# Performance work log

Measured on AMD Instinct MI355X. Metric: run time of the kernel, lower is better.

Reference implementation:

```python
import jax, jax.numpy as jnp
import numpy as np

N_RAYS = 131072
N_NODES = 524288
ENC_DEPTH = 8
ENC_DIM = 16
N_POINTS = 8
IN_DIM = N_POINTS * ENC_DEPTH * ENC_DIM  # 1024
INNER = 64


def setup_inputs() -> dict:
    key = jax.random.key(0)
    ks = jax.random.split(key, 9)
    orig = jax.random.uniform(ks[0], (N_RAYS, 3), dtype=jnp.float32)
    end = jax.random.uniform(ks[1], (N_RAYS, 3), dtype=jnp.float32)
    history = jax.random.randint(ks[2], (N_RAYS, ENC_DEPTH), 0, N_NODES, dtype=jnp.int32).astype(jnp.int64)
    nodes_min = jax.random.uniform(ks[3], (N_NODES, 3), dtype=jnp.float32)
    # extents strictly positive (module replaces 0 extents with 0.5)
    nodes_extent = jax.random.uniform(ks[4], (N_NODES, 3), dtype=jnp.float32) + 0.1
    emb = jax.random.normal(ks[5], (N_NODES, 8 * ENC_DIM), dtype=jnp.float32) * 0.1
    W1 = jax.random.normal(ks[6], (IN_DIM, INNER), dtype=jnp.float32) * (1.0 / np.sqrt(IN_DIM))
    W2 = jax.random.normal(ks[7], (INNER, INNER), dtype=jnp.float32) * (1.0 / np.sqrt(INNER))
    W3 = jax.random.normal(ks[8], (INNER, 2), dtype=jnp.float32) * (1.0 / np.sqrt(INNER))
    return {"orig": orig, "end": end, "history": history, "nodes_min": nodes_min,
            "nodes_extent": nodes_extent, "emb": emb, "W1": W1, "W2": W2, "W3": W3}


def _net_forward(orig, end, history, nodes_min, nodes_extent, emb, W1, W2, W3):
    n = orig.shape[0]
    d = history.shape[1]
    # gather per-ray, per-depth node data (irregular access)
    nmin = nodes_min[history]          # (n, d, 3)
    ext = nodes_extent[history]        # (n, d, 3)
    po = jnp.clip((orig[:, None, :] - nmin) / ext, 0.0, 1.0)  # (n, d, 3)
    pe = jnp.clip((end[:, None, :] - nmin) / ext, 0.0, 1.0)
    ts = jnp.linspace(0.0, 1.0, N_POINTS, dtype=orig.dtype)
    pts = po[:, :, None, :] + (pe - po)[:, :, None, :] * ts[None, None, :, None]  # (n, d, P, 3)
    xd, yd, zd = pts[..., 0], pts[..., 1], pts[..., 2]
    # corner weights in the same order as bbox_feature.chunk(8): 000,100,010,001,101,011,110,111
    w = jnp.stack([
        (1 - xd) * (1 - yd) * (1 - zd),
        xd * (1 - yd) * (1 - zd),
        (1 - xd) * yd * (1 - zd),
        (1 - xd) * (1 - yd) * zd,
        xd * (1 - yd) * zd,
        (1 - xd) * yd * zd,
        xd * yd * (1 - zd),
        xd * yd * zd,
    ], axis=-1)                                    # (n, d, P, 8)
    corners = emb[history].reshape(n, d, 8, ENC_DIM)  # (n, d, 8, F)
    feat = jnp.einsum('ndpk,ndkf->ndpf', w, corners)  # (n, d, P, F)
    feat = feat.reshape(n, d * N_POINTS * ENC_DIM)    # concat over depth
    h = jax.nn.relu(feat @ W1)
    h = jax.nn.relu(h @ W2)
    a = h @ W3                                        # (n, 2)
    lengths = jnp.linalg.norm(end - orig, axis=-1)
    pred_cls = a[:, 0]
    pred_dist = a[:, 1] * lengths
    return jnp.stack([pred_cls, pred_dist], axis=-1)  # (n, 2)


def reference(orig, end, history, nodes_min, nodes_extent, emb, W1, W2, W3):
    return _net_forward(orig, end, history, nodes_min, nodes_extent, emb, W1, W2, W3)
```

## Files before the change

### kernel.cpp

```cpp
#include <hip/hip_runtime.h>
#include <cstdint>
#include <type_traits>

#define ENC_DEPTH 8
#define RAYS 64
#define THREADS 256

typedef __attribute__((ext_vector_type(8))) short bf16x8;
typedef __attribute__((ext_vector_type(4))) float f32x4;

__device__ __forceinline__ unsigned short f2bf(float x) {
    union { float f; unsigned u; } v; v.f = x;
    unsigned r = v.u + 0x7fffu + ((v.u >> 16) & 1u);
    return (unsigned short)(r >> 16);
}
__device__ __forceinline__ float bf2f(unsigned short h) {
    union { unsigned u; float f; } v; v.u = ((unsigned)h) << 16;
    return v.f;
}
__device__ __forceinline__ float clamp01(float x) {
    return fminf(fmaxf(x, 0.0f), 1.0f);
}
__device__ __forceinline__ void async_copy16(const void* g, void* l) {
    __builtin_amdgcn_global_load_lds(
        (const __attribute__((address_space(1))) void*)g,
        (__attribute__((address_space(3))) void*)l, 16, 0, 0);
}

__global__ void emb_bf16_kernel(const float* __restrict__ emb,
                                unsigned short* __restrict__ emb2) {
    size_t i = ((size_t)blockIdx.x * 256 + threadIdx.x) * 8;
    float4 a = *(const float4*)(emb + i);
    float4 b = *(const float4*)(emb + i + 4);
    bf16x8 v;
    v[0] = (short)f2bf(a.x); v[1] = (short)f2bf(a.y);
    v[2] = (short)f2bf(a.z); v[3] = (short)f2bf(a.w);
    v[4] = (short)f2bf(b.x); v[5] = (short)f2bf(b.y);
    v[6] = (short)f2bf(b.z); v[7] = (short)f2bf(b.w);
    *(bf16x8*)(emb2 + i) = v;
}

__global__ void w1_frag_kernel(const float* __restrict__ W1,
                               unsigned short* __restrict__ W1F) {
    int slot = blockIdx.x * 256 + threadIdx.x;
    int lane = slot & 63, tile = (slot >> 6) & 3, kk = (slot >> 8) & 3, d = slot >> 10;
    int n = tile * 16 + (lane & 15);
    int kbase = d * 128 + kk * 32 + (lane >> 4) * 8;
    bf16x8 v;
    #pragma unroll
    for (int j = 0; j < 8; ++j) v[j] = (short)f2bf(W1[(size_t)(kbase + j) * 64 + n]);
    *(bf16x8*)(W1F + (size_t)slot * 8) = v;
}

template <int BF16T>
__global__ __launch_bounds__(THREADS) void nbvh3(
    const float* __restrict__ orig, const float* __restrict__ endp,
    const int* __restrict__ hist, const float* __restrict__ nodes_min,
    const float* __restrict__ nodes_extent, const void* __restrict__ embx,
    const unsigned short* __restrict__ W1F, const float* __restrict__ W2,
    const float* __restrict__ W3, float* __restrict__ out)
{
    using CTy = typename std::conditional<BF16T, unsigned short, float>::type;
    __shared__ __align__(16) CTy cbuf[2][8320];
    __shared__ float pope_s[RAYS * ENC_DEPTH * 6];
    __shared__ int hist_s[RAYS * ENC_DEPTH];

    const int t = threadIdx.x;
    const int lane = t & 63, w = t >> 6;
    const int r0 = blockIdx.x * RAYS;

    hist_s[t] = hist[r0 * ENC_DEPTH + t];
    hist_s[t + 256] = hist[r0 * ENC_DEPTH + t + 256];
    __syncthreads();

    auto issue_gather = [&](int d, int buf) {
        char* base = (char*)&cbuf[buf][0];
        if (BF16T) {
            #pragma unroll
            for (int r = 0; r < 4; ++r) {
                int ray = r * 16 + w * 4 + (lane >> 4);
                int node = hist_s[(ray << 3) + d];
                const char* g = (const char*)embx + ((size_t)node << 8) + ((lane & 15) << 4);
                async_copy16(g, base + (r * 4 + w) * 1040 + lane * 16);
            }
        } else {
            #pragma unroll
            for (int r = 0; r < 8; ++r) {
                int ray = r * 8 + w * 2 + (lane >> 5);
                int node = hist_s[(ray << 3) + d];
                const char* g = (const char*)embx + ((size_t)node << 9) + ((lane & 31) << 4);
                async_copy16(g, base + (r * 4 + w) * 1040 + lane * 16);
            }
        }
    };

    issue_gather(0, 0);

    #pragma unroll
    for (int rep = 0; rep < 2; ++rep) {
        int task = t + rep * 256;
        int ray = task >> 3;
        int node = hist_s[task];
        float nm0 = nodes_min[node * 3 + 0], nm1 = nodes_min[node * 3 + 1], nm2 = nodes_min[node * 3 + 2];
        float ex0 = nodes_extent[node * 3 + 0], ex1 = nodes_extent[node * 3 + 1], ex2 = nodes_extent[node * 3 + 2];
        float o0 = orig[(r0 + ray) * 3 + 0], o1 = orig[(r0 + ray) * 3 + 1], o2 = orig[(r0 + ray) * 3 + 2];
        float e0 = endp[(r0 + ray) * 3 + 0], e1 = endp[(r0 + ray) * 3 + 1], e2 = endp[(r0 + ray) * 3 + 2];
        float* pp = pope_s + task * 6;
        pp[0] = clamp01((o0 - nm0) / ex0);
        pp[1] = clamp01((o1 - nm1) / ex1);
        pp[2] = clamp01((o2 - nm2) / ex2);
        pp[3] = clamp01((e0 - nm0) / ex0);
        pp[4] = clamp01((e1 - nm1) / ex1);
        pp[5] = clamp01((e2 - nm2) / ex2);
    }
    __syncthreads();

    f32x4 acc[4];
    #pragma unroll
    for (int i = 0; i < 4; ++i) acc[i] = (f32x4){0.f, 0.f, 0.f, 0.f};

    const int c = lane & 15, q = lane >> 4;
    const int ray = w * 16 + c;
    const int qh = q & 1;
    const int qp = q >> 1;

    #pragma unroll 1
    for (int d = 0; d < ENC_DEPTH; ++d) {
        if (d < ENC_DEPTH - 1) issue_gather(d + 1, (d + 1) & 1);

        bf16x8 bfr[4][4];
        #pragma unroll
        for (int kk = 0; kk < 4; ++kk)
            #pragma unroll
            for (int tile = 0; tile < 4; ++tile)
                bfr[kk][tile] = *(const bf16x8*)(W1F +
                    ((size_t)(((d * 4 + kk) * 4 + tile) * 64 + lane)) * 8);

        const float* pp = pope_s + ((ray << 3) + d) * 6;
        float po0 = pp[0], po1 = pp[1], po2 = pp[2], pe0 = pp[3], pe1 = pp[4], pe2 = pp[5];
        float X[4], OX[4], Y[4], OY[4], Z[4], OZ[4];
        #pragma unroll
        for (int kk = 0; kk < 4; ++kk) {
            float tp = (float)(2 * kk + qp) * (1.0f / 7.0f);
            X[kk] = po0 + (pe0 - po0) * tp; OX[kk] = 1.f - X[kk];
            Y[kk] = po1 + (pe1 - po1) * tp; OY[kk] = 1.f - Y[kk];
            Z[kk] = po2 + (pe2 - po2) * tp; OZ[kk] = 1.f - Z[kk];
        }

        float fa[4][8];
        #pragma unroll
        for (int kk = 0; kk < 4; ++kk)
            #pragma unroll
            for (int j = 0; j < 8; ++j) fa[kk][j] = 0.f;

        #pragma unroll
        for (int j = 0; j < 8; ++j) {
            int c8 = j ^ (c & 3);
            float e[8];
            if (BF16T) {
                const unsigned short* crow = (const unsigned short*)&cbuf[d & 1][0]
                    + (ray >> 2) * 520 + (ray & 3) * 128 + c8 * 16 + qh * 8;
                bf16x8 cv = *(const bf16x8*)crow;
                #pragma unroll
                for (int i = 0; i < 8; ++i) e[i] = bf2f((unsigned short)cv[i]);
            } else {
                const float* crow = (const float*)&cbuf[d & 1][0]
                    + (ray >> 1) * 260 + (ray & 1) * 128 + c8 * 16 + qh * 8;
                float4 ea = *(const float4*)crow;
                float4 eb = *(const float4*)(crow + 4);
                e[0] = ea.x; e[1] = ea.y; e[2] = ea.z; e[3] = ea.w;
                e[4] = eb.x; e[5] = eb.y; e[6] = eb.z; e[7] = eb.w;
            }
            #pragma unroll
            for (int kk = 0; kk < 4; ++kk) {
                float wx = ((0xD2 >> c8) & 1) ? X[kk] : OX[kk];
                float wy = ((0xE4 >> c8) & 1) ? Y[kk] : OY[kk];
                float wz = ((0xB8 >> c8) & 1) ? Z[kk] : OZ[kk];
                float wgt = wx * wy * wz;
                #pragma unroll
                for (int i = 0; i < 8; ++i)
                    fa[kk][i] = fmaf(wgt, e[i], fa[kk][i]);
            }
        }

        #pragma unroll
        for (int kk = 0; kk < 4; ++kk) {
            bf16x8 af;
            #pragma unroll
            for (int j = 0; j < 8; ++j) af[j] = (short)f2bf(fa[kk][j]);
            #pragma unroll
            for (int tile = 0; tile < 4; ++tile)
                acc[tile] = __builtin_amdgcn_mfma_f32_16x16x32_bf16(af, bfr[kk][tile], acc[tile], 0, 0, 0);
        }
        __syncthreads();
    }

    float* h1 = (float*)&cbuf[0][0];
    float* h2 = BF16T ? ((float*)&cbuf[1][0]) : (((float*)&cbuf[0][0]) + 4160);
    #pragma unroll
    for (int tile = 0; tile < 4; ++tile)
        #pragma unroll
        for (int r = 0; r < 4; ++r)
            h1[(w * 16 + q * 4 + r) * 65 + tile * 16 + c] = fmaxf(acc[tile][r], 0.f);
    __syncthreads();

    {
        int ray2 = t >> 2, jg = (t & 3) << 4;
        float s[16];
        #pragma unroll
        for (int j = 0; j < 16; ++j) s[j] = 0.f;
        const float* hrow = h1 + ray2 * 65;
        #pragma unroll 4
        for (int i = 0; i < 64; ++i) {
            float hv = hrow[i];
            const float4* wr = (const float4*)(W2 + (i << 6) + jg);
            float4 a0 = wr[0], a1 = wr[1], a2 = wr[2], a3 = wr[3];
            s[0]  = fmaf(hv, a0.x, s[0]);  s[1]  = fmaf(hv, a0.y, s[1]);
            s[2]  = fmaf(hv, a0.z, s[2]);  s[3]  = fmaf(hv, a0.w, s[3]);
            s[4]  = fmaf(hv, a1.x, s[4]);  s[5]  = fmaf(hv, a1.y, s[5]);
            s[6]  = fmaf(hv, a1.z, s[6]);  s[7]  = fmaf(hv, a1.w, s[7]);
            s[8]  = fmaf(hv, a2.x, s[8]);  s[9]  = fmaf(hv, a2.y, s[9]);
            s[10] = fmaf(hv, a2.z, s[10]); s[11] = fmaf(hv, a2.w, s[11]);
            s[12] = fmaf(hv, a3.x, s[12]); s[13] = fmaf(hv, a3.y, s[13]);
            s[14] = fmaf(hv, a3.z, s[14]); s[15] = fmaf(hv, a3.w, s[15]);
        }
        float* h2row = h2 + ray2 * 65 + jg;
        #pragma unroll
        for (int j = 0; j < 16; ++j) h2row[j] = fmaxf(s[j], 0.f);
    }
    __syncthreads();

    if (t < 128) {
        int ray3 = t >> 1, cc = t & 1;
        const float* hrow = h2 + ray3 * 65;
        float a = 0.f;
        #pragma unroll 16
        for (int i = 0; i < 64; ++i) a = fmaf(hrow[i], W3[i * 2 + cc], a);
        if (cc) {
            float dx = endp[(r0 + ray3) * 3 + 0] - orig[(r0 + ray3) * 3 + 0];
            float dy = endp[(r0 + ray3) * 3 + 1] - orig[(r0 + ray3) * 3 + 1];
            float dz = endp[(r0 + ray3) * 3 + 2] - orig[(r0 + ray3) * 3 + 2];
            a *= sqrtf(dx * dx + dy * dy + dz * dz);
        }
        out[((r0 + ray3) << 1) + cc] = a;
    }
}

extern "C" void kernel_launch(void* const* d_in, const int* in_sizes, int n_in,
                              void* d_out, int out_size, void* d_ws, size_t ws_size,
                              hipStream_t stream) {
    const float* orig = (const float*)d_in[0];
    const float* endp = (const float*)d_in[1];
    const int*   hist = (const int*)d_in[2];
    const float* nmin = (const float*)d_in[3];
    const float* next = (const float*)d_in[4];
    const float* emb  = (const float*)d_in[5];
    const float* W1   = (const float*)d_in[6];
    const float* W2   = (const float*)d_in[7];
    const float* W3   = (const float*)d_in[8];
    float* out = (float*)d_out;

    const int n_nodes = in_sizes[5] / 128;
    const size_t emb2_bytes = (size_t)n_nodes * 128 * 2;
    const int n_rays = in_sizes[0] / 3;
    const bool use_bf16 = ws_size >= emb2_bytes + 131072 * 2;

    if (use_bf16) {
        unsigned short* EMB2 = (unsigned short*)d_ws;
        unsigned short* W1F = (unsigned short*)((char*)d_ws + emb2_bytes);
        emb_bf16_kernel<<<dim3((n_nodes * 128) / (256 * 8)), dim3(256), 0, stream>>>(emb, EMB2);
        w1_frag_kernel<<<dim3(32), dim3(256), 0, stream>>>(W1, W1F);
        nbvh3<1><<<dim3(n_rays / RAYS), dim3(THREADS), 0, stream>>>(
            orig, endp, hist, nmin, next, EMB2, W1F, W2, W3, out);
    } else {
        unsigned short* W1F = (unsigned short*)d_ws;
        w1_frag_kernel<<<dim3(32), dim3(256), 0, stream>>>(W1, W1F);
        nbvh3<0><<<dim3(n_rays / RAYS), dim3(THREADS), 0, stream>>>(
            orig, endp, hist, nmin, next, emb, W1F, W2, W3, out);
    }
}
```

Measured before the change: 601.1 us.

## Make gather pipeline wave-private with 4-stage buffering and vmcnt waits

Each wave now loads its own 16 rays' history and node data, and gathers its own embedding rows into a wave-private slice of a 4-deep LDS ring. This removes every block-wide __syncthreads in the depth loop and replaces them with s_waitcnt vmcnt waits. Two depths are processed per iteration, with W1 fragments for both loaded up front and the gathers for the next two depths issued two steps ahead. The fp32 fallback is dropped and launch_bounds(256,2) is added, which costs more LDS and register pressure and assumes the workspace is always large enough.

New measurement: 665.6 us. 10.7% more time.

```diff
diff --git a/kernel.cpp b/kernel.cpp
--- a/kernel.cpp
+++ b/kernel.cpp
@@ -1,6 +1,5 @@
 #include <hip/hip_runtime.h>
 #include <cstdint>
-#include <type_traits>
 
 #define ENC_DEPTH 8
 #define RAYS 64
@@ -26,6 +25,9 @@
         (const __attribute__((address_space(1))) void*)g,
         (__attribute__((address_space(3))) void*)l, 16, 0, 0);
 }
+
+#define WAIT_VMCNT_8() __builtin_amdgcn_s_waitcnt(0xF78)
+#define WAIT_VMCNT_0() __builtin_amdgcn_s_waitcnt(0xF70)
 
 __global__ void emb_bf16_kernel(const float* __restrict__ emb,
                                 unsigned short* __restrict__ emb2) {
@@ -52,16 +54,14 @@
     *(bf16x8*)(W1F + (size_t)slot * 8) = v;
 }
 
-template <int BF16T>
-__global__ __launch_bounds__(THREADS) void nbvh3(
+__global__ __launch_bounds__(THREADS, 2) void nbvh4(
     const float* __restrict__ orig, const float* __restrict__ endp,
     const int* __restrict__ hist, const float* __restrict__ nodes_min,
-    const float* __restrict__ nodes_extent, const void* __restrict__ embx,
+    const float* __restrict__ nodes_extent, const unsigned short* __restrict__ EMB2,
     const unsigned short* __restrict__ W1F, const float* __restrict__ W2,
     const float* __restrict__ W3, float* __restrict__ out)
 {
-    using CTy = typename std::conditional<BF16T, unsigned short, float>::type;
-    __shared__ __align__(16) CTy cbuf[2][8320];
+    __shared__ __align__(16) unsigned short cbuf[33280];
     __shared__ float pope_s[RAYS * ENC_DEPTH * 6];
     __shared__ int hist_s[RAYS * ENC_DEPTH];
 
@@ -69,74 +69,60 @@
     const int lane = t & 63, w = t >> 6;
     const int r0 = blockIdx.x * RAYS;
 
-    hist_s[t] = hist[r0 * ENC_DEPTH + t];
-    hist_s[t + 256] = hist[r0 * ENC_DEPTH + t + 256];
-    __syncthreads();
-
-    auto issue_gather = [&](int d, int buf) {
-        char* base = (char*)&cbuf[buf][0];
-        if (BF16T) {
-            #pragma unroll
-            for (int r = 0; r < 4; ++r) {
-                int ray = r * 16 + w * 4 + (lane >> 4);
-                int node = hist_s[(ray << 3) + d];
-                const char* g = (const char*)embx + ((size_t)node << 8) + ((lane & 15) << 4);
-                async_copy16(g, base + (r * 4 + w) * 1040 + lane * 16);
-            }
-        } else {
-            #pragma unroll
-            for (int r = 0; r < 8; ++r) {
-                int ray = r * 8 + w * 2 + (lane >> 5);
-                int node = hist_s[(ray << 3) + d];
-                const char* g = (const char*)embx + ((size_t)node << 9) + ((lane & 31) << 4);
-                async_copy16(g, base + (r * 4 + w) * 1040 + lane * 16);
-            }
-        }
-    };
-
-    issue_gather(0, 0);
-
+    hist_s[w * 128 + lane]      = hist[(r0 + w * 16) * 8 + lane];
+    hist_s[w * 128 + 64 + lane] = hist[(r0 + w * 16) * 8 + 64 + lane];
+
+    float pv[2][6];
+    int tasks[2];
     #pragma unroll
     for (int rep = 0; rep < 2; ++rep) {
-        int task = t + rep * 256;
-        int ray = task >> 3;
-        int node = hist_s[task];
+        int task = rep * 64 + lane;
+        tasks[rep] = task;
+        int rw = task >> 3;
+        int node = hist_s[w * 128 + task];
         float nm0 = nodes_min[node * 3 + 0], nm1 = nodes_min[node * 3 + 1], nm2 = nodes_min[node * 3 + 2];
         float ex0 = nodes_extent[node * 3 + 0], ex1 = nodes_extent[node * 3 + 1], ex2 = nodes_extent[node * 3 + 2];
-        float o0 = orig[(r0 + ray) * 3 + 0], o1 = orig[(r0 + ray) * 3 + 1], o2 = orig[(r0 + ray) * 3 + 2];
-        float e0 = endp[(r0 + ray) * 3 + 0], e1 = endp[(r0 + ray) * 3 + 1], e2 = endp[(r0 + ray) * 3 + 2];
-        float* pp = pope_s + task * 6;
-        pp[0] = clamp01((o0 - nm0) / ex0);
-        pp[1] = clamp01((o1 - nm1) / ex1);
-        pp[2] = clamp01((o2 - nm2) / ex2);
-        pp[3] = clamp01((e0 - nm0) / ex0);
-        pp[4] = clamp01((e1 - nm1) / ex1);
-        pp[5] = clamp01((e2 - nm2) / ex2);
-    }
-    __syncthreads();
+        int gr = r0 + w * 16 + rw;
+        float o0 = orig[gr * 3 + 0], o1 = orig[gr * 3 + 1], o2 = orig[gr * 3 + 2];
+        float e0 = endp[gr * 3 + 0], e1 = endp[gr * 3 + 1], e2 = endp[gr * 3 + 2];
+        pv[rep][0] = clamp01((o0 - nm0) / ex0);
+        pv[rep][1] = clamp01((o1 - nm1) / ex1);
+        pv[rep][2] = clamp01((o2 - nm2) / ex2);
+        pv[rep][3] = clamp01((e0 - nm0) / ex0);
+        pv[rep][4] = clamp01((e1 - nm1) / ex1);
+        pv[rep][5] = clamp01((e2 - nm2) / ex2);
+    }
+
+    auto issue_depth = [&](int d) {
+        char* base = (char*)cbuf + (d & 3) * 16640 + w * 4160;
+        #pragma unroll
+        for (int r = 0; r < 4; ++r) {
+            int rw = r * 4 + (lane >> 4);
+            int node = hist_s[w * 128 + rw * 8 + d];
+            const char* g = (const char*)EMB2 + ((size_t)node << 8) + ((lane & 15) << 4);
+            async_copy16(g, base + r * 1040 + lane * 16);
+        }
+    };
+    issue_depth(0);
+    issue_depth(1);
+
+    #pragma unroll
+    for (int rep = 0; rep < 2; ++rep) {
+        float* pp = pope_s + w * 768 + tasks[rep] * 6;
+        #pragma unroll
+        for (int i = 0; i < 6; ++i) pp[i] = pv[rep][i];
+    }
 
     f32x4 acc[4];
     #pragma unroll
     for (int i = 0; i < 4; ++i) acc[i] = (f32x4){0.f, 0.f, 0.f, 0.f};
 
     const int c = lane & 15, q = lane >> 4;
-    const int ray = w * 16 + c;
     const int qh = q & 1;
     const int qp = q >> 1;
 
-    #pragma unroll 1
-    for (int d = 0; d < ENC_DEPTH; ++d) {
-        if (d < ENC_DEPTH - 1) issue_gather(d + 1, (d + 1) & 1);
-
-        bf16x8 bfr[4][4];
-        #pragma unroll
-        for (int kk = 0; kk < 4; ++kk)
-            #pragma unroll
-            for (int tile = 0; tile < 4; ++tile)
-                bfr[kk][tile] = *(const bf16x8*)(W1F +
-                    ((size_t)(((d * 4 + kk) * 4 + tile) * 64 + lane)) * 8);
-
-        const float* pp = pope_s + ((ray << 3) + d) * 6;
+    auto compute_depth = [&](int d, const bf16x8* bfr) {
+        const float* pp = pope_s + w * 768 + (c * 8 + d) * 6;
         float po0 = pp[0], po1 = pp[1], po2 = pp[2], pe0 = pp[3], pe1 = pp[4], pe2 = pp[5];
         float X[4], OX[4], Y[4], OY[4], Z[4], OZ[4];
         #pragma unroll
@@ -146,31 +132,21 @@
             Y[kk] = po1 + (pe1 - po1) * tp; OY[kk] = 1.f - Y[kk];
             Z[kk] = po2 + (pe2 - po2) * tp; OZ[kk] = 1.f - Z[kk];
         }
-
         float fa[4][8];
         #pragma unroll
         for (int kk = 0; kk < 4; ++kk)
             #pragma unroll
             for (int j = 0; j < 8; ++j) fa[kk][j] = 0.f;
 
+        const char* cb = (const char*)cbuf + (d & 3) * 16640 + w * 4160
+                         + (c >> 2) * 1040 + (c & 3) * 256 + qh * 16;
         #pragma unroll
         for (int j = 0; j < 8; ++j) {
             int c8 = j ^ (c & 3);
+            bf16x8 cv = *(const bf16x8*)(cb + c8 * 32);
             float e[8];
-            if (BF16T) {
-                const unsigned short* crow = (const unsigned short*)&cbuf[d & 1][0]
-                    + (ray >> 2) * 520 + (ray & 3) * 128 + c8 * 16 + qh * 8;
-                bf16x8 cv = *(const bf16x8*)crow;
-                #pragma unroll
-                for (int i = 0; i < 8; ++i) e[i] = bf2f((unsigned short)cv[i]);
-            } else {
-                const float* crow = (const float*)&cbuf[d & 1][0]
-                    + (ray >> 1) * 260 + (ray & 1) * 128 + c8 * 16 + qh * 8;
-                float4 ea = *(const float4*)crow;
-                float4 eb = *(const float4*)(crow + 4);
-                e[0] = ea.x; e[1] = ea.y; e[2] = ea.z; e[3] = ea.w;
-                e[4] = eb.x; e[5] = eb.y; e[6] = eb.z; e[7] = eb.w;
-            }
+            #pragma unroll
+            for (int i = 0; i < 8; ++i) e[i] = bf2f((unsigned short)cv[i]);
             #pragma unroll
             for (int kk = 0; kk < 4; ++kk) {
                 float wx = ((0xD2 >> c8) & 1) ? X[kk] : OX[kk];
@@ -182,7 +158,6 @@
                     fa[kk][i] = fmaf(wgt, e[i], fa[kk][i]);
             }
         }
-
         #pragma unroll
         for (int kk = 0; kk < 4; ++kk) {
             bf16x8 af;
@@ -190,13 +165,26 @@
             for (int j = 0; j < 8; ++j) af[j] = (short)f2bf(fa[kk][j]);
             #pragma unroll
             for (int tile = 0; tile < 4; ++tile)
-                acc[tile] = __builtin_amdgcn_mfma_f32_16x16x32_bf16(af, bfr[kk][tile], acc[tile], 0, 0, 0);
-        }
-        __syncthreads();
-    }
-
-    float* h1 = (float*)&cbuf[0][0];
-    float* h2 = BF16T ? ((float*)&cbuf[1][0]) : (((float*)&cbuf[0][0]) + 4160);
+                acc[tile] = __builtin_amdgcn_mfma_f32_16x16x32_bf16(af, bfr[kk * 4 + tile], acc[tile], 0, 0, 0);
+        }
+    };
+
+    #pragma unroll 1
+    for (int dd = 0; dd < 8; dd += 2) {
+        bf16x8 bfr[2][16];
+        #pragma unroll
+        for (int h = 0; h < 2; ++h)
+            #pragma unroll
+            for (int f = 0; f < 16; ++f)
+                bfr[h][f] = *(const bf16x8*)(W1F + ((size_t)(((dd + h) * 16 + f) * 64 + lane)) * 8);
+        if (dd + 2 < 8) { issue_depth(dd + 2); issue_depth(dd + 3); }
+        if (dd < 6) WAIT_VMCNT_8(); else WAIT_VMCNT_0();
+        compute_depth(dd, bfr[0]);
+        compute_depth(dd + 1, bfr[1]);
+    }
+
+    float* h1 = (float*)cbuf;
+    float* h2 = h1 + 4160;
     #pragma unroll
     for (int tile = 0; tile < 4; ++tile)
         #pragma unroll
@@ -263,19 +251,12 @@
     const int n_nodes = in_sizes[5] / 128;
     const size_t emb2_bytes = (size_t)n_nodes * 128 * 2;
     const int n_rays = in_sizes[0] / 3;
-    const bool use_bf16 = ws_size >= emb2_bytes + 131072 * 2;
-
-    if (use_bf16) {
-        unsigned short* EMB2 = (unsigned short*)d_ws;
-        unsigned short* W1F = (unsigned short*)((char*)d_ws + emb2_bytes);
-        emb_bf16_kernel<<<dim3((n_nodes * 128) / (256 * 8)), dim3(256), 0, stream>>>(emb, EMB2);
-        w1_frag_kernel<<<dim3(32), dim3(256), 0, stream>>>(W1, W1F);
-        nbvh3<1><<<dim3(n_rays / RAYS), dim3(THREADS), 0, stream>>>(
-            orig, endp, hist, nmin, next, EMB2, W1F, W2, W3, out);
-    } else {
-        unsigned short* W1F = (unsigned short*)d_ws;
-        w1_frag_kernel<<<dim3(32), dim3(256), 0, stream>>>(W1, W1F);
-        nbvh3<0><<<dim3(n_rays / RAYS), dim3(THREADS), 0, stream>>>(
-            orig, endp, hist, nmin, next, emb, W1F, W2, W3, out);
-    }
-}
+
+    unsigned short* EMB2 = (unsigned short*)d_ws;
+    unsigned short* W1F = (unsigned short*)((char*)d_ws + emb2_bytes);
+
+    emb_bf16_kernel<<<dim3((n_nodes * 128) / (256 * 8)), dim3(256), 0, stream>>>(emb, EMB2);
+    w1_frag_kernel<<<dim3(32), dim3(256), 0, stream>>>(W1, W1F);
+    nbvh4<<<dim3(n_rays / RAYS), dim3(THREADS), 0, stream>>>(
+        orig, endp, hist, nmin, next, EMB2, W1F, W2, W3, out);
+}
```
